# Kernel optimization log

Hardware: AMD Instinct MI355X
Metric: run time of the kernel (lower is better)

## Reference

```python
import jax, jax.numpy as jnp
import numpy as np

TAU = 0.5
LAM = 0.5
EPS = 1e-8


def setup_inputs() -> dict:
    key = jax.random.key(0)
    ks = jax.random.split(key, 4)
    N, D = 10000, 8
    z_mp = jax.random.normal(ks[0], (N, D), dtype=jnp.float32)
    z_sc = jax.random.normal(ks[1], (N, D), dtype=jnp.float32)
    # xavier_normal with gain=1.414 for an 8x8 linear: std = gain*sqrt(2/(fan_in+fan_out))
    std = 1.414 * np.sqrt(2.0 / (D + D))
    W1 = jax.random.normal(ks[2], (D, D), dtype=jnp.float32) * std
    W2 = jax.random.normal(ks[3], (D, D), dtype=jnp.float32) * std
    b1 = jnp.zeros((D,), dtype=jnp.float32)
    b2 = jnp.zeros((D,), dtype=jnp.float32)
    return {"z_mp": z_mp, "z_sc": z_sc, "W1": W1, "b1": b1, "W2": W2, "b2": b2}


def _proj(z, W1, b1, W2, b2):
    h = jax.nn.elu(z @ W1.T + b1)
    return h @ W2.T + b2


def reference(z_mp, z_sc, W1, b1, W2, b2):
    zp1 = _proj(z_mp, W1, b1, W2, b2)  # [N, D]
    zp2 = _proj(z_sc, W1, b1, W2, b2)  # [N, D]
    n1 = jnp.linalg.norm(zp1, axis=-1, keepdims=True)  # [N, 1]
    n2 = jnp.linalg.norm(zp2, axis=-1, keepdims=True)  # [N, 1]
    # cosine-sim logits scaled by tau, exponentiated: [N, N]
    m = jnp.exp((zp1 @ zp2.T) / (n1 * n2.T) / TAU)
    diag = jnp.diagonal(m)  # shared by both directions (m.T has same diag)
    row_sum = jnp.sum(m, axis=1) + EPS   # mp->sc direction
    col_sum = jnp.sum(m, axis=0) + EPS   # sc->mp direction (row-sum of m.T)
    lori_mp = -jnp.mean(jnp.log(diag / row_sum))
    lori_sc = -jnp.mean(jnp.log(diag / col_sum))
    return LAM * lori_mp + (1.0 - LAM) * lori_sc
```

## Files before the change

kernel.cpp:

```cpp
#include <hip/hip_runtime.h>

#define D 8
#define EPS 1e-8f
#define LOG2E_OVER_TAU 2.8853900817779268f
#define LN2 0.6931471805599453f

#define NPAD 10240
#define WR 8
#define ROWS_PER_WAVE (WR * 16)
#define ROWS_PER_BLOCK (ROWS_PER_WAVE * 4)
#define JS 64

using f16x8 = __attribute__((ext_vector_type(8))) _Float16;
using f32x4 = __attribute__((ext_vector_type(4))) float;

__device__ __forceinline__ float fast_exp2(float x) {
    return __builtin_amdgcn_exp2f(x);
}

__global__ void proj_kernel(const float* __restrict__ z1f,
                            const float* __restrict__ z2f,
                            const float* __restrict__ W1f,
                            const float* __restrict__ b1f,
                            const float* __restrict__ W2f,
                            const float* __restrict__ b2f,
                            f16x8* __restrict__ Ah, f16x8* __restrict__ Al,
                            f16x8* __restrict__ Bh, f16x8* __restrict__ Bl,
                            float* __restrict__ ldiag,
                            float* __restrict__ rs,
                            float* __restrict__ cs,
                            float* __restrict__ out,
                            int N) {
    int n = blockIdx.x * blockDim.x + threadIdx.x;
    if (n >= NPAD) return;
    rs[n] = 0.f;
    cs[n] = 0.f;
    if (n == 0) out[0] = 0.f;

    if (n >= N) {
        f16x8 z = {(_Float16)0.f, (_Float16)0.f, (_Float16)0.f, (_Float16)0.f,
                   (_Float16)0.f, (_Float16)0.f, (_Float16)0.f, (_Float16)0.f};
        Ah[n] = z; Al[n] = z; Bh[n] = z; Bl[n] = z;
        return;
    }

    float W1[D][D], W2[D][D], B1[D], B2[D];
#pragma unroll
    for (int k = 0; k < D; ++k) {
        B1[k] = b1f[k];
        B2[k] = b2f[k];
#pragma unroll
        for (int d2 = 0; d2 < D; ++d2) {
            W1[k][d2] = W1f[k * D + d2];
            W2[k][d2] = W2f[k * D + d2];
        }
    }

    const float4* z1v = (const float4*)z1f + 2 * n;
    const float4* z2v = (const float4*)z2f + 2 * n;
    float4 r1a = z1v[0], r1b = z1v[1];
    float4 r2a = z2v[0], r2b = z2v[1];
    float z1[D] = {r1a.x, r1a.y, r1a.z, r1a.w, r1b.x, r1b.y, r1b.z, r1b.w};
    float z2[D] = {r2a.x, r2a.y, r2a.z, r2a.w, r2b.x, r2b.y, r2b.z, r2b.w};

    float h1[D], h2[D];
#pragma unroll
    for (int k = 0; k < D; ++k) {
        float t1 = B1[k], t2 = B1[k];
#pragma unroll
        for (int d2 = 0; d2 < D; ++d2) {
            t1 = fmaf(z1[d2], W1[k][d2], t1);
            t2 = fmaf(z2[d2], W1[k][d2], t2);
        }
        h1[k] = (t1 > 0.f) ? t1 : (expf(t1) - 1.f);
        h2[k] = (t2 > 0.f) ? t2 : (expf(t2) - 1.f);
    }

    float p1[D], p2[D];
    float sq1 = 0.f, sq2 = 0.f;
#pragma unroll
    for (int o = 0; o < D; ++o) {
        float t1 = B2[o], t2 = B2[o];
#pragma unroll
        for (int k = 0; k < D; ++k) {
            t1 = fmaf(h1[k], W2[o][k], t1);
            t2 = fmaf(h2[k], W2[o][k], t2);
        }
        p1[o] = t1; p2[o] = t2;
        sq1 = fmaf(t1, t1, sq1);
        sq2 = fmaf(t2, t2, sq2);
    }
    float s1 = LOG2E_OVER_TAU * rsqrtf(sq1);
    float s2 = rsqrtf(sq2);

    f16x8 ah, al, bh, bl;
    float dacc = 0.f;
#pragma unroll
    for (int o = 0; o < D; ++o) {
        float av = p1[o] * s1;
        float bv = p2[o] * s2;
        dacc = fmaf(av, bv, dacc);
        _Float16 avh = (_Float16)av;
        _Float16 bvh = (_Float16)bv;
        ah[o] = avh;
        al[o] = (_Float16)(av - (float)avh);
        bh[o] = bvh;
        bl[o] = (_Float16)(bv - (float)bvh);
    }
    Ah[n] = ah; Al[n] = al; Bh[n] = bh; Bl[n] = bl;
    ldiag[n] = dacc * LN2;
}

__global__ __launch_bounds__(256) void pair_mfma_kernel(
        const f16x8* __restrict__ Ah, const f16x8* __restrict__ Al,
        const f16x8* __restrict__ Bh, const f16x8* __restrict__ Bl,
        float* __restrict__ rs,
        float* __restrict__ cs,
        int N, int nJT, int jtPerBlock) {
    int tid = threadIdx.x;
    int lane = tid & 63;
    int wave = tid >> 6;
    int c = lane & 15;
    int g = lane >> 4;
    int wbase = blockIdx.x * ROWS_PER_BLOCK + wave * ROWS_PER_WAVE;
    if (wbase >= N) return;

    int invi = wbase + ROWS_PER_WAVE - N;
    if (invi < 0) invi = 0;
    float inv = (float)invi;

    f16x8 kz = {(_Float16)0.f, (_Float16)0.f, (_Float16)0.f, (_Float16)0.f,
                (_Float16)0.f, (_Float16)0.f, (_Float16)0.f, (_Float16)0.f};

    const f16x8* Asrc = (g == 1) ? Al : Ah;
    f16x8 afrag[WR];
#pragma unroll
    for (int t = 0; t < WR; ++t) {
        afrag[t] = Asrc[wbase + t * 16 + c];
        if (g == 3) afrag[t] = kz;
    }

    float rsacc[WR][4];
#pragma unroll
    for (int t = 0; t < WR; ++t)
#pragma unroll
        for (int r = 0; r < 4; ++r) rsacc[t][r] = 0.f;

    int jt0 = blockIdx.y * jtPerBlock;
    int jt1 = min(nJT, jt0 + jtPerBlock);

    const f16x8* Bsrc = (g == 2) ? Bl : Bh;
    f32x4 czero = {0.f, 0.f, 0.f, 0.f};

    f16x8 bcur = kz;
    if (g != 3) bcur = Bsrc[jt0 * 16 + c];

    for (int jt = jt0; jt < jt1; ++jt) {
        f16x8 bnext = bcur;
        if (jt + 1 < jt1 && g != 3) bnext = Bsrc[(jt + 1) * 16 + c];

        float csum = 0.f;
#pragma unroll
        for (int t = 0; t < WR; ++t) {
            f32x4 dv = __builtin_amdgcn_mfma_f32_16x16x32_f16(
                afrag[t], bcur, czero, 0, 0, 0);
#pragma unroll
            for (int r = 0; r < 4; ++r) {
                float e = fast_exp2(dv[r]);
                rsacc[t][r] += e;
                csum += e;
            }
        }
        csum += __shfl_xor(csum, 16, 64);
        csum += __shfl_xor(csum, 32, 64);
        if (g == 0) atomicAdd(&cs[jt * 16 + c], csum - inv);

        bcur = bnext;
    }

#pragma unroll
    for (int t = 0; t < WR; ++t) {
#pragma unroll
        for (int r = 0; r < 4; ++r) {
            float v = rsacc[t][r];
            v += __shfl_xor(v, 1, 64);
            v += __shfl_xor(v, 2, 64);
            v += __shfl_xor(v, 4, 64);
            v += __shfl_xor(v, 8, 64);
            int row = wbase + t * 16 + g * 4 + r;
            if (c == 0 && row < N) atomicAdd(&rs[row], v);
        }
    }
}

__global__ void finalize_kernel(const float* __restrict__ rs,
                                const float* __restrict__ cs,
                                const float* __restrict__ ldiag,
                                float* __restrict__ out,
                                int N) {
    int gid = blockIdx.x * blockDim.x + threadIdx.x;
    int stride = gridDim.x * blockDim.x;
    float acc = 0.f;
    for (int i = gid; i < N; i += stride) {
        acc += 0.5f * __logf(rs[i] + EPS) + 0.5f * __logf(cs[i] + EPS) - ldiag[i];
    }
#pragma unroll
    for (int off = 32; off > 0; off >>= 1)
        acc += __shfl_down(acc, off, 64);
    __shared__ float wsum[4];
    int wave = threadIdx.x >> 6;
    if ((threadIdx.x & 63) == 0) wsum[wave] = acc;
    __syncthreads();
    if (threadIdx.x == 0) {
        float total = wsum[0] + wsum[1] + wsum[2] + wsum[3];
        atomicAdd(out, total / (float)N);
    }
}

extern "C" void kernel_launch(void* const* d_in, const int* in_sizes, int n_in,
                              void* d_out, int out_size, void* d_ws, size_t ws_size,
                              hipStream_t stream) {
    const float* z1 = (const float*)d_in[0];
    const float* z2 = (const float*)d_in[1];
    const float* W1 = (const float*)d_in[2];
    const float* b1 = (const float*)d_in[3];
    const float* W2 = (const float*)d_in[4];
    const float* b2 = (const float*)d_in[5];
    int N = in_sizes[0] / D;

    f16x8* Ah = (f16x8*)d_ws;
    f16x8* Al = Ah + NPAD;
    f16x8* Bh = Al + NPAD;
    f16x8* Bl = Bh + NPAD;
    float* ldiag = (float*)(Bl + NPAD);
    float* rs = ldiag + NPAD;
    float* cs = rs + NPAD;
    float* out = (float*)d_out;

    proj_kernel<<<NPAD / 256, 256, 0, stream>>>(z1, z2, W1, b1, W2, b2,
                                                Ah, Al, Bh, Bl,
                                                ldiag, rs, cs, out, N);

    int iBlocks = NPAD / ROWS_PER_BLOCK;
    int nJT = N / 16;
    int jtPerBlock = (nJT + JS - 1) / JS;
    dim3 pgrid(iBlocks, JS);
    pair_mfma_kernel<<<pgrid, 256, 0, stream>>>(Ah, Al, Bh, Bl, rs, cs,
                                                N, nJT, jtPerBlock);

    finalize_kernel<<<10, 256, 0, stream>>>(rs, cs, ldiag, out, N);
}
```

Baseline: 99.42 us.

## Fuse finalize into pair kernel via last-block counter and LDS column-sum reduction

Column sums from the four waves of a block are now staged in shared memory and combined before one global atomic per column, which cuts global atomic traffic by four. The separate finalize kernel is removed. The last block to finish, found with an atomic done counter, computes the log-sum reduction and writes the output. This saves a kernel launch and its drain gap, at the cost of extra barriers, threadfences, and a serial tail handled by a single block.

```diff
diff --git a/kernel.cpp b/kernel.cpp
--- a/kernel.cpp
+++ b/kernel.cpp
@@ -10,6 +10,7 @@
 #define ROWS_PER_WAVE (WR * 16)
 #define ROWS_PER_BLOCK (ROWS_PER_WAVE * 4)
 #define JS 64
+#define JTPB_MAX 10
 
 using f16x8 = __attribute__((ext_vector_type(8))) _Float16;
 using f32x4 = __attribute__((ext_vector_type(4))) float;
@@ -30,12 +31,13 @@
                             float* __restrict__ rs,
                             float* __restrict__ cs,
                             float* __restrict__ out,
+                            unsigned* __restrict__ done_ctr,
                             int N) {
     int n = blockIdx.x * blockDim.x + threadIdx.x;
     if (n >= NPAD) return;
     rs[n] = 0.f;
     cs[n] = 0.f;
-    if (n == 0) out[0] = 0.f;
+    if (n == 0) { out[0] = 0.f; done_ctr[0] = 0u; }
 
     if (n >= N) {
         f16x8 z = {(_Float16)0.f, (_Float16)0.f, (_Float16)0.f, (_Float16)0.f,
@@ -114,19 +116,26 @@
 __global__ __launch_bounds__(256) void pair_mfma_kernel(
         const f16x8* __restrict__ Ah, const f16x8* __restrict__ Al,
         const f16x8* __restrict__ Bh, const f16x8* __restrict__ Bl,
+        const float* __restrict__ ldiag,
         float* __restrict__ rs,
         float* __restrict__ cs,
+        float* __restrict__ out,
+        unsigned* __restrict__ done_ctr,
         int N, int nJT, int jtPerBlock) {
+    __shared__ float cs_lds[4][JTPB_MAX * 16];
+    __shared__ float wsum[4];
+    __shared__ int lastFlag;
+
     int tid = threadIdx.x;
     int lane = tid & 63;
     int wave = tid >> 6;
     int c = lane & 15;
     int g = lane >> 4;
     int wbase = blockIdx.x * ROWS_PER_BLOCK + wave * ROWS_PER_WAVE;
-    if (wbase >= N) return;
 
     int invi = wbase + ROWS_PER_WAVE - N;
     if (invi < 0) invi = 0;
+    if (invi > ROWS_PER_WAVE) invi = ROWS_PER_WAVE;
     float inv = (float)invi;
 
     f16x8 kz = {(_Float16)0.f, (_Float16)0.f, (_Float16)0.f, (_Float16)0.f,
@@ -148,12 +157,13 @@
 
     int jt0 = blockIdx.y * jtPerBlock;
     int jt1 = min(nJT, jt0 + jtPerBlock);
+    int jtCount = jt1 - jt0; if (jtCount < 0) jtCount = 0;
 
     const f16x8* Bsrc = (g == 2) ? Bl : Bh;
     f32x4 czero = {0.f, 0.f, 0.f, 0.f};
 
     f16x8 bcur = kz;
-    if (g != 3) bcur = Bsrc[jt0 * 16 + c];
+    if (jtCount > 0 && g != 3) bcur = Bsrc[jt0 * 16 + c];
 
     for (int jt = jt0; jt < jt1; ++jt) {
         f16x8 bnext = bcur;
@@ -173,47 +183,59 @@
         }
         csum += __shfl_xor(csum, 16, 64);
         csum += __shfl_xor(csum, 32, 64);
-        if (g == 0) atomicAdd(&cs[jt * 16 + c], csum - inv);
+        if (g == 0) cs_lds[wave][(jt - jt0) * 16 + c] = csum - inv;
 
         bcur = bnext;
     }
 
-#pragma unroll
-    for (int t = 0; t < WR; ++t) {
-#pragma unroll
-        for (int r = 0; r < 4; ++r) {
-            float v = rsacc[t][r];
-            v += __shfl_xor(v, 1, 64);
-            v += __shfl_xor(v, 2, 64);
-            v += __shfl_xor(v, 4, 64);
-            v += __shfl_xor(v, 8, 64);
-            int row = wbase + t * 16 + g * 4 + r;
-            if (c == 0 && row < N) atomicAdd(&rs[row], v);
-        }
-    }
-}
-
-__global__ void finalize_kernel(const float* __restrict__ rs,
-                                const float* __restrict__ cs,
-                                const float* __restrict__ ldiag,
-                                float* __restrict__ out,
-                                int N) {
-    int gid = blockIdx.x * blockDim.x + threadIdx.x;
-    int stride = gridDim.x * blockDim.x;
-    float acc = 0.f;
-    for (int i = gid; i < N; i += stride) {
-        acc += 0.5f * __logf(rs[i] + EPS) + 0.5f * __logf(cs[i] + EPS) - ldiag[i];
-    }
-#pragma unroll
-    for (int off = 32; off > 0; off >>= 1)
-        acc += __shfl_down(acc, off, 64);
-    __shared__ float wsum[4];
-    int wave = threadIdx.x >> 6;
-    if ((threadIdx.x & 63) == 0) wsum[wave] = acc;
     __syncthreads();
-    if (threadIdx.x == 0) {
-        float total = wsum[0] + wsum[1] + wsum[2] + wsum[3];
-        atomicAdd(out, total / (float)N);
+    int nEnt = jtCount * 16;
+    for (int e = tid; e < nEnt; e += 256) {
+        float v = cs_lds[0][e] + cs_lds[1][e] + cs_lds[2][e] + cs_lds[3][e];
+        atomicAdd(&cs[jt0 * 16 + e], v);
+    }
+
+    if (jtCount > 0) {
+#pragma unroll
+        for (int t = 0; t < WR; ++t) {
+#pragma unroll
+            for (int r = 0; r < 4; ++r) {
+                float v = rsacc[t][r];
+                v += __shfl_xor(v, 1, 64);
+                v += __shfl_xor(v, 2, 64);
+                v += __shfl_xor(v, 4, 64);
+                v += __shfl_xor(v, 8, 64);
+                int row = wbase + t * 16 + g * 4 + r;
+                if (c == 0 && row < N) atomicAdd(&rs[row], v);
+            }
+        }
+    }
+
+    __threadfence();
+    __syncthreads();
+    if (tid == 0) {
+        unsigned total = gridDim.x * gridDim.y;
+        unsigned prev = atomicAdd(done_ctr, 1u);
+        lastFlag = (prev == total - 1u);
+    }
+    __syncthreads();
+    if (lastFlag) {
+        __threadfence();
+        float acc = 0.f;
+        for (int i = tid; i < N; i += 256) {
+            float rv = __hip_atomic_load(&rs[i], __ATOMIC_RELAXED,
+                                         __HIP_MEMORY_SCOPE_AGENT);
+            float cv = __hip_atomic_load(&cs[i], __ATOMIC_RELAXED,
+                                         __HIP_MEMORY_SCOPE_AGENT);
+            acc += 0.5f * __logf(rv + EPS) + 0.5f * __logf(cv + EPS) - ldiag[i];
+        }
+#pragma unroll
+        for (int off = 32; off > 0; off >>= 1)
+            acc += __shfl_down(acc, off, 64);
+        if ((tid & 63) == 0) wsum[tid >> 6] = acc;
+        __syncthreads();
+        if (tid == 0)
+            out[0] = (wsum[0] + wsum[1] + wsum[2] + wsum[3]) / (float)N;
     }
 }
 
@@ -235,18 +257,20 @@
     float* ldiag = (float*)(Bl + NPAD);
     float* rs = ldiag + NPAD;
     float* cs = rs + NPAD;
+    unsigned* done_ctr = (unsigned*)(cs + NPAD);
     float* out = (float*)d_out;
 
     proj_kernel<<<NPAD / 256, 256, 0, stream>>>(z1, z2, W1, b1, W2, b2,
                                                 Ah, Al, Bh, Bl,
-                                                ldiag, rs, cs, out, N);
+                                                ldiag, rs, cs, out, done_ctr, N);
 
     int iBlocks = NPAD / ROWS_PER_BLOCK;
     int nJT = N / 16;
     int jtPerBlock = (nJT + JS - 1) / JS;
-    dim3 pgrid(iBlocks, JS);
-    pair_mfma_kernel<<<pgrid, 256, 0, stream>>>(Ah, Al, Bh, Bl, rs, cs,
+    if (jtPerBlock > JTPB_MAX) jtPerBlock = JTPB_MAX;
+    int yBlocks = (nJT + jtPerBlock - 1) / jtPerBlock;
+    dim3 pgrid(iBlocks, yBlocks);
+    pair_mfma_kernel<<<pgrid, 256, 0, stream>>>(Ah, Al, Bh, Bl, ldiag,
+                                                rs, cs, out, done_ctr,
                                                 N, nJT, jtPerBlock);
-
-    finalize_kernel<<<10, 256, 0, stream>>>(rs, cs, ldiag, out, N);
-}
+}
```

After: 170.3 us. +71.3%, slower.

## Reduce column sums through LDS per block and shrink j-tiles per block

Applied to the files above, without the earlier changes.

Each block now handles a fixed 5 column tiles, so the grid grows from 64 to 125 y-blocks. Per-tile column partial sums from all waves and lane groups are staged in shared memory and reduced after a barrier, giving one global atomic per column per block instead of one per wave per tile. Padded-row corrections move to block level. Waves past N no longer exit early, so the barrier is safe, but they do redundant zero work, and the code assumes nJT is divisible by JTPB.

```diff
diff --git a/kernel.cpp b/kernel.cpp
--- a/kernel.cpp
+++ b/kernel.cpp
@@ -9,7 +9,7 @@
 #define WR 8
 #define ROWS_PER_WAVE (WR * 16)
 #define ROWS_PER_BLOCK (ROWS_PER_WAVE * 4)
-#define JS 64
+#define JTPB 5
 
 using f16x8 = __attribute__((ext_vector_type(8))) _Float16;
 using f32x4 = __attribute__((ext_vector_type(4))) float;
@@ -116,18 +116,21 @@
         const f16x8* __restrict__ Bh, const f16x8* __restrict__ Bl,
         float* __restrict__ rs,
         float* __restrict__ cs,
-        int N, int nJT, int jtPerBlock) {
+        int N, int nJT) {
+    __shared__ float cs_lds[16][JTPB * 16];
+
     int tid = threadIdx.x;
     int lane = tid & 63;
     int wave = tid >> 6;
     int c = lane & 15;
     int g = lane >> 4;
-    int wbase = blockIdx.x * ROWS_PER_BLOCK + wave * ROWS_PER_WAVE;
-    if (wbase >= N) return;
-
-    int invi = wbase + ROWS_PER_WAVE - N;
-    if (invi < 0) invi = 0;
-    float inv = (float)invi;
+    int bbase = blockIdx.x * ROWS_PER_BLOCK;
+    int wbase = bbase + wave * ROWS_PER_WAVE;
+
+    int binv = bbase + ROWS_PER_BLOCK - N;
+    if (binv < 0) binv = 0;
+    if (binv > ROWS_PER_BLOCK) binv = ROWS_PER_BLOCK;
+    float blockInv = (float)binv;
 
     f16x8 kz = {(_Float16)0.f, (_Float16)0.f, (_Float16)0.f, (_Float16)0.f,
                 (_Float16)0.f, (_Float16)0.f, (_Float16)0.f, (_Float16)0.f};
@@ -146,8 +149,7 @@
 #pragma unroll
         for (int r = 0; r < 4; ++r) rsacc[t][r] = 0.f;
 
-    int jt0 = blockIdx.y * jtPerBlock;
-    int jt1 = min(nJT, jt0 + jtPerBlock);
+    int jt0 = blockIdx.y * JTPB;
 
     const f16x8* Bsrc = (g == 2) ? Bl : Bh;
     f32x4 czero = {0.f, 0.f, 0.f, 0.f};
@@ -155,9 +157,9 @@
     f16x8 bcur = kz;
     if (g != 3) bcur = Bsrc[jt0 * 16 + c];
 
-    for (int jt = jt0; jt < jt1; ++jt) {
+    for (int q = 0; q < JTPB; ++q) {
         f16x8 bnext = bcur;
-        if (jt + 1 < jt1 && g != 3) bnext = Bsrc[(jt + 1) * 16 + c];
+        if (q + 1 < JTPB && g != 3) bnext = Bsrc[(jt0 + q + 1) * 16 + c];
 
         float csum = 0.f;
 #pragma unroll
@@ -171,11 +173,18 @@
                 csum += e;
             }
         }
-        csum += __shfl_xor(csum, 16, 64);
-        csum += __shfl_xor(csum, 32, 64);
-        if (g == 0) atomicAdd(&cs[jt * 16 + c], csum - inv);
+        cs_lds[wave * 4 + g][q * 16 + c] = csum;
 
         bcur = bnext;
+    }
+
+    __syncthreads();
+    int nEnt = JTPB * 16;
+    for (int e = tid; e < nEnt; e += 256) {
+        float v = 0.f;
+#pragma unroll
+        for (int s = 0; s < 16; ++s) v += cs_lds[s][e];
+        atomicAdd(&cs[jt0 * 16 + e], v - blockInv);
     }
 
 #pragma unroll
@@ -243,10 +252,10 @@
 
     int iBlocks = NPAD / ROWS_PER_BLOCK;
     int nJT = N / 16;
-    int jtPerBlock = (nJT + JS - 1) / JS;
-    dim3 pgrid(iBlocks, JS);
+    int yBlocks = nJT / JTPB;
+    dim3 pgrid(iBlocks, yBlocks);
     pair_mfma_kernel<<<pgrid, 256, 0, stream>>>(Ah, Al, Bh, Bl, rs, cs,
-                                                N, nJT, jtPerBlock);
+                                                N, nJT);
 
     finalize_kernel<<<10, 256, 0, stream>>>(rs, cs, ldiag, out, N);
 }
```

Result: slower. 111.4 us (+12.0%).
